# Kernel optimization log

Hardware: AMD Instinct MI355X
Metric: run time of the kernel (lower is better)

Reference implementation:

```python
import jax, jax.numpy as jnp
import numpy as np

N, C, H, W = 8, 3, 720, 1280


def setup_inputs() -> dict:
    key = jax.random.key(0)
    k1, k2 = jax.random.split(key)
    image = jax.random.normal(k1, (N, C, H, W), dtype=jnp.float32)
    # scale flow so integer truncation gives real displacements (and collisions)
    flow = jax.random.normal(k2, (N, 2, H, W), dtype=jnp.float32) * 20.0
    return {"image": image, "flow": flow}


def _warp_fw(image, flow):
    n, c, h, w = image.shape
    hw = h * w
    # flat source mesh coordinates (same for all batches)
    mx = jnp.broadcast_to(jnp.arange(w, dtype=jnp.int32)[None, :], (h, w)).reshape(-1)
    my = jnp.broadcast_to(jnp.arange(h, dtype=jnp.int32)[:, None], (h, w)).reshape(-1)
    fx = flow[:, 0].reshape(n, hw)
    fy = flow[:, 1].reshape(n, hw)
    # torch .long() truncates toward zero; astype(int32) matches
    wx = jnp.clip(mx[None, :] + fx.astype(jnp.int32), 0, w - 1)
    wy = jnp.clip(my[None, :] + fy.astype(jnp.int32), 0, h - 1)
    tgt = wy * w + wx  # (n, hw) linear target index
    v = fx * fx + fy * fy
    sortidx = jnp.argsort(v, axis=1)  # (n, hw) ascending
    ranks = jnp.arange(hw, dtype=jnp.int32)

    def per_batch(sortidx_i, tgt_i):
        # rank[p] = position of source pixel p in the sorted write order
        rank = jnp.zeros((hw,), jnp.int32).at[sortidx_i].set(ranks)
        # winning (max) rank at each target location; -1 = hole
        best = jnp.full((hw,), -1, jnp.int32).at[tgt_i].max(rank)
        covered = best >= 0
        # winning source pixel index = sortidx[best_rank]
        src = jnp.take(sortidx_i, jnp.clip(best, 0, hw - 1))
        return src, covered

    src, covered = jax.vmap(per_batch)(sortidx, tgt)  # (n, hw) each
    img_flat = image.reshape(n, c, hw)
    gathered = jnp.take_along_axis(
        img_flat, jnp.broadcast_to(src[:, None, :], (n, c, hw)), axis=2
    )
    out = jnp.where(covered[:, None, :], gathered, 0.0)
    return out.reshape(n, c, h, w)


def reference(image, flow):
    return _warp_fw(image, flow)
```

## Files before the change

### kernel.cpp

```cpp
#include <hip/hip_runtime.h>
#include <cstdint>

constexpr int N_ = 8;
constexpr int C_ = 3;
constexpr int H_ = 720;
constexpr int W_ = 1280;
constexpr int HW = H_ * W_;

constexpr int TW = 128;
constexpr int TH = 64;
constexpr int M_ = 64;
constexpr int NTX = W_ / TW;
constexpr int NTY = (H_ + TH - 1) / TH;
constexpr int BLK = 1024;
constexpr int OSEG = 16384;
constexpr int SCAP = 128;
constexpr int CSTRIDE = 16;
constexpr int BPB = HW / 1024;

constexpr int NSWEEP = (TH + 2 * M_) / (BLK / 64);

typedef float vf4 __attribute__((ext_vector_type(4)));

struct Outlier { unsigned long long key; int tgt; int pad; };

__device__ __forceinline__ unsigned long long make_key(float fx, float fy, int p) {
    float v = __fadd_rn(__fmul_rn(fx, fx), __fmul_rn(fy, fy));
    return ((unsigned long long)__float_as_uint(v) << 32) | (unsigned int)(p + 1);
}

__global__ __launch_bounds__(256) void outlier_kernel(
    const float* __restrict__ flow,
    unsigned long long* __restrict__ ocnt,
    Outlier* __restrict__ olist) {
    __shared__ unsigned int bcnt;
    __shared__ unsigned long long gbase;
    __shared__ unsigned long long skey[SCAP];
    __shared__ int stgt[SCAP];
    if (threadIdx.x == 0) bcnt = 0;
    __syncthreads();

    int n  = blockIdx.x / BPB;
    int p0 = (blockIdx.x - n * BPB) * 1024 + threadIdx.x * 4;
    const float* f = flow + (size_t)n * 2 * HW;
    vf4 fx4 = *(const vf4*)(f + p0);
    vf4 fy4 = *(const vf4*)(f + HW + p0);
    float fxs[4] = {fx4.x, fx4.y, fx4.z, fx4.w};
    float fys[4] = {fy4.x, fy4.y, fy4.z, fy4.w};
    int y = p0 / W_;
    int x0 = p0 - y * W_;
    #pragma unroll
    for (int i = 0; i < 4; ++i) {
        int dx = (int)fxs[i];
        int dy = (int)fys[i];
        if (dx > M_ || dx < -M_ || dy > M_ || dy < -M_) {
            int wx = min(max(x0 + i + dx, 0), W_ - 1);
            int wy = min(max(y + dy, 0), H_ - 1);
            unsigned long long key = make_key(fxs[i], fys[i], p0 + i);
            int tgt = wy * W_ + wx;
            unsigned int s = atomicAdd(&bcnt, 1u);
            if (s < (unsigned)SCAP) {
                skey[s] = key; stgt[s] = tgt;
            } else {
                unsigned long long o = atomicAdd(&ocnt[(size_t)n * CSTRIDE], 1ULL);
                if (o < (unsigned long long)OSEG) {
                    Outlier e; e.key = key; e.tgt = tgt; e.pad = 0;
                    olist[n * OSEG + (int)o] = e;
                }
            }
        }
    }
    __syncthreads();
    unsigned int c = bcnt > (unsigned)SCAP ? (unsigned)SCAP : bcnt;
    if (threadIdx.x == 0)
        gbase = c ? atomicAdd(&ocnt[(size_t)n * CSTRIDE], (unsigned long long)c)
                  : 0ULL;
    __syncthreads();
    for (unsigned int i = threadIdx.x; i < c; i += 256) {
        unsigned long long o = gbase + i;
        if (o < (unsigned long long)OSEG) {
            Outlier e; e.key = skey[i]; e.tgt = stgt[i]; e.pad = 0;
            olist[n * OSEG + (int)o] = e;
        }
    }
}

__global__ __launch_bounds__(BLK, 8) void warp_tile_kernel(
    const float* __restrict__ image,
    const float* __restrict__ flow,
    const unsigned long long* __restrict__ ocnt,
    const Outlier* __restrict__ olist,
    float* __restrict__ out) {
    __shared__ unsigned long long lkey[TH * TW];
    int bid = blockIdx.x;
    int n    = bid & 7;
    int tile = bid >> 3;
    int tyi = tile / NTX;
    int txi = tile - tyi * NTX;
    int tx0 = txi * TW;
    int ty0 = tyi * TH;
    int th_eff = min(TH, H_ - ty0);
    int tid = threadIdx.x;

    {
        ulonglong2 z; z.x = 0ULL; z.y = 0ULL;
        ulonglong2* l2p = (ulonglong2*)lkey;
        #pragma unroll
        for (int i = 0; i < (TH * TW) / 2 / BLK; ++i)
            l2p[tid + i * BLK] = z;
    }
    __syncthreads();

    {
        unsigned long long craw = ocnt[(size_t)n * CSTRIDE];
        int cnt = (int)(craw > (unsigned long long)OSEG ? OSEG : craw);
        const Outlier* seg = olist + n * OSEG;
        for (int o = tid; o < cnt; o += BLK) {
            Outlier e = seg[o];
            int ey = e.tgt / W_, ex = e.tgt - ey * W_;
            int lx = ex - tx0, ly = ey - ty0;
            if ((unsigned)lx < (unsigned)TW && (unsigned)ly < (unsigned)th_eff)
                atomicMax(&lkey[ly * TW + lx], e.key);
        }
    }

    const float* fx_p = flow + (size_t)n * 2 * HW;
    const float* fy_p = fx_p + HW;
    int x4   = tx0 - M_ + ((tid & 63) << 2);
    int yv0  = ty0 - M_ + (tid >> 6);
    bool xok = (unsigned)x4 < (unsigned)W_;
    #pragma unroll 4
    for (int s = 0; s < NSWEEP; ++s) {
        int y = yv0 + s * 16;
        if (xok && (unsigned)y < (unsigned)H_) {
            int pbase = y * W_ + x4;
            vf4 fx4 = *(const vf4*)(fx_p + pbase);
            vf4 fy4 = *(const vf4*)(fy_p + pbase);
            float fxs[4] = {fx4.x, fx4.y, fx4.z, fx4.w};
            float fys[4] = {fy4.x, fy4.y, fy4.z, fy4.w};
            #pragma unroll
            for (int i = 0; i < 4; ++i) {
                float fx = fxs[i], fy = fys[i];
                int wx = x4 + i + (int)fx;
                int wy = y + (int)fy;
                wx = min(max(wx, 0), W_ - 1);
                wy = min(max(wy, 0), H_ - 1);
                int lx = wx - tx0, ly = wy - ty0;
                if ((unsigned)lx < (unsigned)TW && (unsigned)ly < (unsigned)th_eff) {
                    atomicMax(&lkey[ly * TW + lx], make_key(fx, fy, pbase + i));
                }
            }
        }
    }
    __syncthreads();

    const float* img_n = image + (size_t)n * C_ * HW;
    float* out_n = out + (size_t)n * C_ * HW;
    int q4 = th_eff * (TW / 4);
    for (int s = tid; s < q4; s += BLK) {
        int r = s >> 5;
        int cg = s & 31;
        int lp = r * TW + cg * 4;
        unsigned long long k0 = lkey[lp],     k1 = lkey[lp + 1];
        unsigned long long k2 = lkey[lp + 2], k3 = lkey[lp + 3];
        int s0 = (int)(unsigned int)(k0 & 0xffffffffULL) - 1;
        int s1 = (int)(unsigned int)(k1 & 0xffffffffULL) - 1;
        int s2 = (int)(unsigned int)(k2 & 0xffffffffULL) - 1;
        int s3 = (int)(unsigned int)(k3 & 0xffffffffULL) - 1;
        int op = (ty0 + r) * W_ + tx0 + cg * 4;
        #pragma unroll
        for (int c = 0; c < C_; ++c) {
            const float* pl = img_n + (size_t)c * HW;
            vf4 o;
            o.x = k0 ? pl[s0] : 0.0f;
            o.y = k1 ? pl[s1] : 0.0f;
            o.z = k2 ? pl[s2] : 0.0f;
            o.w = k3 ? pl[s3] : 0.0f;
            __builtin_nontemporal_store(o, (vf4*)(out_n + (size_t)c * HW + op));
        }
    }
}

extern "C" void kernel_launch(void* const* d_in, const int* in_sizes, int n_in,
                              void* d_out, int out_size, void* d_ws, size_t ws_size,
                              hipStream_t stream) {
    const float* image = (const float*)d_in[0];
    const float* flow  = (const float*)d_in[1];
    float* out = (float*)d_out;

    unsigned long long* ocnt = (unsigned long long*)d_ws;
    Outlier* olist = (Outlier*)((char*)d_ws + 1024);

    (void)hipMemsetAsync(ocnt, 0, 1024, stream);

    int k0_blocks = (N_ * HW / 4) / 256;
    outlier_kernel<<<k0_blocks, 256, 0, stream>>>(flow, ocnt, olist);

    warp_tile_kernel<<<N_ * NTX * NTY, BLK, 0, stream>>>(
        image, flow, ocnt, olist, out);
}
```

Baseline: 289.2 us.

## Replace tiled shared-memory warp with global atomicMax scatter plus gather

When the workspace can hold a full per-pixel 64-bit key buffer, the code memsets that buffer, scatters each source pixel's (|flow|^2, index) key into global memory with atomicMax, and then gathers image values in a second kernel. This drops the halo re-reading of flow and the outlier list that the tiled LDS kernel needed. In exchange it adds a ~59MB memset, random global 64-bit atomics and a second pass over the keys. The old tiled path is kept as a fallback when the workspace is too small.

```diff
diff --git a/kernel.cpp b/kernel.cpp
--- a/kernel.cpp
+++ b/kernel.cpp
@@ -6,6 +6,68 @@
 constexpr int H_ = 720;
 constexpr int W_ = 1280;
 constexpr int HW = H_ * W_;
+
+typedef float vf4 __attribute__((ext_vector_type(4)));
+
+__device__ __forceinline__ unsigned long long make_key(float fx, float fy, int p) {
+    float v = __fadd_rn(__fmul_rn(fx, fx), __fmul_rn(fy, fy));
+    return ((unsigned long long)__float_as_uint(v) << 32) | (unsigned int)(p + 1);
+}
+
+constexpr int SBLK = 1024;
+constexpr int CHUNK = SBLK * 4;
+constexpr int NCHUNK = HW / CHUNK;
+
+__global__ __launch_bounds__(SBLK) void scatter_kernel(
+    const float* __restrict__ flow,
+    unsigned long long* __restrict__ keys) {
+    int n     = blockIdx.x & 7;
+    int chunk = blockIdx.x >> 3;
+    int p0 = chunk * CHUNK + (int)threadIdx.x * 4;
+    const float* f = flow + (size_t)n * 2 * HW;
+    vf4 fx4 = *(const vf4*)(f + p0);
+    vf4 fy4 = *(const vf4*)(f + HW + p0);
+    unsigned long long* kb = keys + (size_t)n * HW;
+    int y  = p0 / W_;
+    int x0 = p0 - y * W_;
+    float fxs[4] = {fx4.x, fx4.y, fx4.z, fx4.w};
+    float fys[4] = {fy4.x, fy4.y, fy4.z, fy4.w};
+    #pragma unroll
+    for (int i = 0; i < 4; ++i) {
+        int wx = min(max(x0 + i + (int)fxs[i], 0), W_ - 1);
+        int wy = min(max(y + (int)fys[i], 0), H_ - 1);
+        atomicMax(&kb[wy * W_ + wx], make_key(fxs[i], fys[i], p0 + i));
+    }
+}
+
+__global__ __launch_bounds__(SBLK) void gather_kernel(
+    const float* __restrict__ image,
+    const unsigned long long* __restrict__ keys,
+    float* __restrict__ out) {
+    int n     = blockIdx.x & 7;
+    int chunk = blockIdx.x >> 3;
+    int p0 = chunk * CHUNK + (int)threadIdx.x * 4;
+    const unsigned long long* kb = keys + (size_t)n * HW + p0;
+    ulonglong2 ka = *(const ulonglong2*)(kb);
+    ulonglong2 kc = *(const ulonglong2*)(kb + 2);
+    unsigned long long k0 = ka.x, k1 = ka.y, k2 = kc.x, k3 = kc.y;
+    int s0 = (int)(unsigned int)(k0 & 0xffffffffULL) - 1;
+    int s1 = (int)(unsigned int)(k1 & 0xffffffffULL) - 1;
+    int s2 = (int)(unsigned int)(k2 & 0xffffffffULL) - 1;
+    int s3 = (int)(unsigned int)(k3 & 0xffffffffULL) - 1;
+    const float* img_n = image + (size_t)n * C_ * HW;
+    float* out_n = out + (size_t)n * C_ * HW + p0;
+    #pragma unroll
+    for (int c = 0; c < C_; ++c) {
+        const float* pl = img_n + (size_t)c * HW;
+        vf4 o;
+        o.x = k0 ? pl[s0] : 0.0f;
+        o.y = k1 ? pl[s1] : 0.0f;
+        o.z = k2 ? pl[s2] : 0.0f;
+        o.w = k3 ? pl[s3] : 0.0f;
+        __builtin_nontemporal_store(o, (vf4*)(out_n + (size_t)c * HW));
+    }
+}
 
 constexpr int TW = 128;
 constexpr int TH = 64;
@@ -17,17 +79,9 @@
 constexpr int SCAP = 128;
 constexpr int CSTRIDE = 16;
 constexpr int BPB = HW / 1024;
-
 constexpr int NSWEEP = (TH + 2 * M_) / (BLK / 64);
 
-typedef float vf4 __attribute__((ext_vector_type(4)));
-
 struct Outlier { unsigned long long key; int tgt; int pad; };
-
-__device__ __forceinline__ unsigned long long make_key(float fx, float fy, int p) {
-    float v = __fadd_rn(__fmul_rn(fx, fx), __fmul_rn(fy, fy));
-    return ((unsigned long long)__float_as_uint(v) << 32) | (unsigned int)(p + 1);
-}
 
 __global__ __launch_bounds__(256) void outlier_kernel(
     const float* __restrict__ flow,
@@ -188,14 +242,19 @@
     const float* flow  = (const float*)d_in[1];
     float* out = (float*)d_out;
 
-    unsigned long long* ocnt = (unsigned long long*)d_ws;
-    Outlier* olist = (Outlier*)((char*)d_ws + 1024);
-
-    (void)hipMemsetAsync(ocnt, 0, 1024, stream);
-
-    int k0_blocks = (N_ * HW / 4) / 256;
-    outlier_kernel<<<k0_blocks, 256, 0, stream>>>(flow, ocnt, olist);
-
-    warp_tile_kernel<<<N_ * NTX * NTY, BLK, 0, stream>>>(
-        image, flow, ocnt, olist, out);
-}
+    size_t keys_bytes = (size_t)N_ * HW * 8;
+    if (ws_size >= keys_bytes) {
+        unsigned long long* keys = (unsigned long long*)d_ws;
+        (void)hipMemsetAsync(keys, 0, keys_bytes, stream);
+        scatter_kernel<<<N_ * NCHUNK, SBLK, 0, stream>>>(flow, keys);
+        gather_kernel<<<N_ * NCHUNK, SBLK, 0, stream>>>(image, keys, out);
+    } else {
+        unsigned long long* ocnt = (unsigned long long*)d_ws;
+        Outlier* olist = (Outlier*)((char*)d_ws + 1024);
+        (void)hipMemsetAsync(ocnt, 0, 1024, stream);
+        int k0_blocks = (N_ * HW / 4) / 256;
+        outlier_kernel<<<k0_blocks, 256, 0, stream>>>(flow, ocnt, olist);
+        warp_tile_kernel<<<N_ * NTX * NTY, BLK, 0, stream>>>(
+            image, flow, ocnt, olist, out);
+    }
+}
```

Result: slower. 540.1 us (+86.8%).
